# Kernel optimization log

Hardware: AMD Instinct MI355X
Metric: run time of the kernel (lower is better)

The kernel has to match this reference:

```python
import jax, jax.numpy as jnp
import numpy as np

N = 64
NUM_INPUTS = 6
NUM_OUTPUTS = 2
T_STEPS = 1024
BATCH = 1024
DT = 1.0
TAU = 10.0
ALPHA = DT / TAU
SIGMA_REC = 0.03
SIGMA_INP = 0.03
SLOPE = 1.0  # activation_slope for relu


def setup_inputs() -> dict:
    key = jax.random.key(0)
    k_u, k_rn, k_in, k_wi, k_wr, k_wo = jax.random.split(key, 6)
    u = jax.random.normal(k_u, (NUM_INPUTS, T_STEPS, BATCH), dtype=jnp.float32)
    rec_noise = jax.random.normal(k_rn, (N, T_STEPS, BATCH), dtype=jnp.float32)
    inp_noise = jax.random.normal(k_in, (NUM_INPUTS, T_STEPS, BATCH), dtype=jnp.float32)
    # learned params (masks are all-ones, already folded in)
    W_inp = jax.random.normal(k_wi, (N, NUM_INPUTS), dtype=jnp.float32) * 0.3
    W_rec = jax.random.normal(k_wr, (N, N), dtype=jnp.float32) * (0.9 / np.sqrt(N))
    W_out = jax.random.normal(k_wo, (NUM_OUTPUTS, N), dtype=jnp.float32) * 0.3
    return {"u": u, "rec_noise": rec_noise, "inp_noise": inp_noise,
            "W_inp": W_inp, "W_rec": W_rec, "W_out": W_out}


def _forward(u, rec_noise, inp_noise, W_inp, W_rec, W_out):
    # scale standard-normal noise exactly as torch: sqrt(2/alpha * sigma^2) * randn
    rn = jnp.sqrt(2.0 / ALPHA) * SIGMA_REC * rec_noise   # (N, T, B)
    inn = jnp.sqrt(2.0 / ALPHA) * SIGMA_INP * inp_noise  # (num_inputs, T, B)
    # move to (T, B, feat) for scan
    u_t = jnp.transpose(u, (1, 2, 0))     # (T, B, num_inputs)
    rn_t = jnp.transpose(rn, (1, 2, 0))   # (T, B, N)
    inn_t = jnp.transpose(inn, (1, 2, 0)) # (T, B, num_inputs)
    x0 = jnp.zeros((BATCH, N), dtype=u.dtype)  # self.x = zeros(N), broadcast over batch

    def step(x, inp):
        u_i, rn_i, in_i = inp
        pre = x @ W_rec.T + (u_i + in_i) @ W_inp.T
        act = jnp.maximum(0.0, SLOPE * pre)
        x_new = (1.0 - ALPHA) * x + ALPHA * (act + rn_i)
        return x_new, x_new

    # the torch loop runs T_steps-1 iterations using inputs at steps 0..T-2
    _, xs = jax.lax.scan(step, x0, (u_t[:-1], rn_t[:-1], inn_t[:-1]))
    states_tbn = jnp.concatenate([x0[None], xs], axis=0)  # (T, B, N)
    outputs_tbo = states_tbn @ W_out.T                    # (T, B, num_outputs)
    states = jnp.transpose(states_tbn, (2, 0, 1))   # (N, T, B)
    outputs = jnp.transpose(outputs_tbo, (2, 0, 1)) # (num_outputs, T, B)
    return states, outputs


def reference(u, rec_noise, inp_noise, W_inp, W_rec, W_out):
    return _forward(u, rec_noise, inp_noise, W_inp, W_rec, W_out)
```

## Files before the change

kernel.cpp:

```cpp
#include <hip/hip_runtime.h>

#define NN 64
#define NI 6
#define TT 1024
#define BB 1024
#define TB (TT * BB)
#define NSCALE 0.13416407864998738f
#define ARNSCALE 0.013416407864998739f
#define RREC 72
#define BSTRIDE (TT * RREC)

__device__ __forceinline__ float rdlane(float v, int l) {
    return __int_as_float(__builtin_amdgcn_readlane(__float_as_int(v), l));
}

__global__ __launch_bounds__(256) void build_rnu(
    const float* __restrict__ u,
    const float* __restrict__ rn,
    const float* __restrict__ inn,
    float* __restrict__ rnu)
{
    const int blk = blockIdx.x;
    const int t   = blk >> 4;
    const int b0  = (blk & 15) * 64;
    const int tid = threadIdx.x;

    __shared__ float lds[64][65];

    {
        const int c  = tid & 63;
        const int r0 = tid >> 6;
#pragma unroll
        for (int it = 0; it < 16; ++it) {
            const int n = 4 * it + r0;
            lds[c][n] = ARNSCALE * rn[n * TB + t * BB + b0 + c];
        }
    }
    __syncthreads();
    {
        const int cn = tid & 63;
        const int r0 = tid >> 6;
#pragma unroll
        for (int it = 0; it < 16; ++it) {
            const int r = 4 * it + r0;
            rnu[(b0 + r) * BSTRIDE + t * RREC + cn] = lds[r][cn];
        }
    }
    {
        const int i  = tid & 7;
        const int br = tid >> 3;
#pragma unroll
        for (int it = 0; it < 2; ++it) {
            const int b = br + 32 * it;
            float v = 0.0f;
            if (i < NI) {
                const int g = i * TB + t * BB + b0 + b;
                v = fmaf(NSCALE, inn[g], u[g]);
            }
            rnu[(b0 + b) * BSTRIDE + t * RREC + 64 + i] = v;
        }
    }
}

__global__ __launch_bounds__(64) void latent_rnn_lds(
    const float* __restrict__ rn_in,
    float* __restrict__ x_out,
    const float* __restrict__ Winp,
    const float* __restrict__ Wrec)
{
    const int hw = blockIdx.x;
    const int b  = (hw & 7) * 128 + (hw >> 3);
    const int n  = threadIdx.x;

    __shared__ __align__(16) float xs[2][80];

    float w[72];
#pragma unroll
    for (int k = 0; k < NN; k += 4) {
        const float4 w4 = *reinterpret_cast<const float4*>(Wrec + n * NN + k);
        w[k] = w4.x; w[k + 1] = w4.y; w[k + 2] = w4.z; w[k + 3] = w4.w;
    }
#pragma unroll
    for (int i = 0; i < NI; ++i) w[64 + i] = Winp[n * NI + i];
    w[70] = 0.0f; w[71] = 0.0f;

    const float* rptr = rn_in + b * BSTRIDE + n;
    const float* uptr = rn_in + b * BSTRIDE + 64 + (n & 7);
    float*       xdst = x_out + b * BSTRIDE + n;

    xs[0][n] = 0.0f;
    if (n < 8) xs[0][64 + n] = uptr[0];

    float rnb[4], utb[4];
#pragma unroll
    for (int d = 0; d < 4; ++d) {
        rnb[d] = rptr[d * RREC];
        utb[d] = uptr[(d + 1) * RREC];
    }

    float xreg = 0.0f;

#define STEP(tcur, slot, P)                                                   \
    do {                                                                      \
        const float rcur = rnb[slot];                                         \
        const float ucur = utb[slot];                         \
        { const int tp = ((tcur) + 4 < TT - 2) ? (tcur) + 4 : TT - 2;         \
          rnb[slot] = rptr[tp * RREC]; }                                      \
        { const int tq = ((tcur) + 5 < TT - 2) ? (tcur) + 5 : TT - 2;         \
          utb[slot] = uptr[tq * RREC]; }                                      \
        \
        const float4* row = reinterpret_cast<const float4*>(&xs[P][0]);       \
        float a0 = 0.f, a1 = 0.f, a2 = 0.f, a3 = 0.f;                         \
        _Pragma("unroll")                                                     \
        for (int q = 0; q < 18; ++q) {                                        \
            const float4 v = row[q];                                          \
            a0 = fmaf(v.x, w[4 * q + 0], a0);                                 \
            a1 = fmaf(v.y, w[4 * q + 1], a1);                                 \
            a2 = fmaf(v.z, w[4 * q + 2], a2);                                 \
            a3 = fmaf(v.w, w[4 * q + 3], a3);                                 \
        }                                                                     \
        const float pre = (a0 + a1) + (a2 + a3);                              \
        const float xn  = fmaf(0.9f, xreg,                                    \
                               fmaf(0.1f, fmaxf(pre, 0.f), rcur));            \
        xreg = xn;                                                            \
        xs[(P) ^ 1][n] = xn;                        \
        if (n < 8) xs[(P) ^ 1][64 + n] = ucur;                \
        xdst[(tcur) * RREC] = xn;                    \
    } while (0)

#pragma unroll 1
    for (int t = 0; t < 1020; t += 4) {
        STEP(t + 0, 0, 0);
        STEP(t + 1, 1, 1);
        STEP(t + 2, 2, 0);
        STEP(t + 3, 3, 1);
    }
    STEP(1020, 0, 0);
    STEP(1021, 1, 1);
    STEP(1022, 2, 0);
#undef STEP
}

__global__ __launch_bounds__(256) void trans_out(
    const float* __restrict__ rnu,
    const float* __restrict__ Wout,
    float* __restrict__ states,
    float* __restrict__ outputs)
{
    const int blk = blockIdx.x;
    const int t   = blk >> 4;
    const int b0  = (blk & 15) * 64;
    const int tid = threadIdx.x;

    __shared__ float xt[64][65];
    __shared__ float wo[2][64];

    if (tid < 128) wo[tid >> 6][tid & 63] = Wout[tid];

    const int col = tid & 63;
    const int r0  = tid >> 6;
    if (t == 0) {
#pragma unroll
        for (int it = 0; it < 16; ++it) xt[4 * it + r0][col] = 0.0f;
    } else {
#pragma unroll
        for (int it = 0; it < 16; ++it) {
            const int r = 4 * it + r0;
            xt[r][col] = rnu[(b0 + r) * BSTRIDE + (t - 1) * RREC + col];
        }
    }
    __syncthreads();

#pragma unroll
    for (int it = 0; it < 16; ++it) {
        const int n = 4 * it + r0;
        states[n * TB + t * BB + b0 + col] = xt[col][n];
    }

    if (tid < 128) {
        const int o  = tid >> 6;
        const int bb = tid & 63;
        float acc = 0.0f;
#pragma unroll
        for (int k = 0; k < NN; ++k) acc = fmaf(xt[bb][k], wo[o][k], acc);
        outputs[o * TB + t * BB + b0 + bb] = acc;
    }
}

#define BARRIER() do {                                                        \
    __builtin_amdgcn_sched_barrier(0);                                        \
    asm volatile("s_waitcnt lgkmcnt(0)\n\ts_barrier" ::: "memory");           \
    __builtin_amdgcn_sched_barrier(0);                                        \
} while (0)

__global__ __launch_bounds__(256, 1) void latent_rnn_fb(
    const float* __restrict__ u, const float* __restrict__ rn,
    const float* __restrict__ inn, const float* __restrict__ Winp,
    const float* __restrict__ Wrec, float* __restrict__ states)
{
    const int hw  = blockIdx.x;
    const int lb  = (hw & 7) * 32 + (hw >> 3);
    const int b0  = lb * 4;
    const int tid = threadIdx.x;
    const int l   = tid & 63;
    const int w   = tid >> 6;
    const int n   = tid >> 2;
    const int bs  = tid & 3;

    __shared__ float rnT[2][NN][5];
    __shared__ float xT[2][NN][5];
    __shared__ float iT[2][4][8];

    float wreg[NN];
#pragma unroll
    for (int k = 0; k < NN; k += 4) {
        const float4 w4 = *reinterpret_cast<const float4*>(Wrec + l * NN + k);
        wreg[k] = w4.x; wreg[k+1] = w4.y; wreg[k+2] = w4.z; wreg[k+3] = w4.w;
    }
    float wi[NI];
#pragma unroll
    for (int i = 0; i < NI; ++i) wi[i] = Winp[l * NI + i];

    const float* rsrc = rn + n * TB + b0 + bs;
    float*       sdst = states + n * TB + b0 + bs;
    const bool  ist  = (tid < NI * 4);
    const int   ii   = tid >> 2;
    const int   ib   = tid & 3;
    const float* usrc = u   + ii * TB + b0 + ib;
    const float* isrc = inn + ii * TB + b0 + ib;

    rnT[0][n][bs] = rsrc[0];
    if (ist) iT[0][ib][ii] = fmaf(NSCALE, isrc[0], usrc[0]);
    xT[0][l][w] = 0.0f;

    float rnPF[4], uPF[4], iPF[4];
#pragma unroll
    for (int d = 0; d < 4; ++d) {
        rnPF[d] = rsrc[(d + 1) * BB];
        if (ist) { uPF[d] = usrc[(d + 1) * BB]; iPF[d] = isrc[(d + 1) * BB]; }
    }
    __syncthreads();

    float xreg = 0.0f;

#define FSTEP(tcur, slot, CC)                                                 \
  {                                                                           \
    sdst[(tcur) * BB] = xT[CC][n][bs];                                        \
    const float rcur = rnT[CC][l][w];                                         \
    const float4 iv0 = *reinterpret_cast<const float4*>(&iT[CC][w][0]);       \
    const float2 iv1 = *reinterpret_cast<const float2*>(&iT[CC][w][4]);       \
    float a0 = 0.f, a1 = 0.f, a2 = 0.f, a3 = 0.f;                             \
    _Pragma("unroll")                                                         \
    for (int k = 0; k < NN; k += 4) {                                         \
        a0 = fmaf(rdlane(xreg, k + 0), wreg[k + 0], a0);                      \
        a1 = fmaf(rdlane(xreg, k + 1), wreg[k + 1], a1);                      \
        a2 = fmaf(rdlane(xreg, k + 2), wreg[k + 2], a2);                      \
        a3 = fmaf(rdlane(xreg, k + 3), wreg[k + 3], a3);                      \
    }                                                                         \
    a0 = fmaf(iv0.x, wi[0], a0); a1 = fmaf(iv0.y, wi[1], a1);                 \
    a2 = fmaf(iv0.z, wi[2], a2); a3 = fmaf(iv0.w, wi[3], a3);                 \
    a0 = fmaf(iv1.x, wi[4], a0); a1 = fmaf(iv1.y, wi[5], a1);                 \
    const float pre = (a0 + a1) + (a2 + a3);                                  \
    const float xn  = fmaf(0.9f, xreg,                                        \
                           fmaf(0.1f, fmaxf(pre, 0.f), ARNSCALE * rcur));     \
    xreg = xn;                                                                \
    xT[(CC) ^ 1][l][w] = xn;                                                  \
    rnT[(CC) ^ 1][n][bs] = rnPF[slot];                                        \
    if (ist) iT[(CC) ^ 1][ib][ii] = fmaf(NSCALE, iPF[slot], uPF[slot]);       \
    { int tp = (tcur) + 5; if (tp > TT - 2) tp = TT - 2;                      \
      rnPF[slot] = rsrc[tp * BB];                                             \
      if (ist) { uPF[slot] = usrc[tp * BB]; iPF[slot] = isrc[tp * BB]; } }    \
    BARRIER();                                                                \
  }

#pragma unroll 1
    for (int t = 0; t < 1020; t += 4) {
        FSTEP(t + 0, 0, 0);
        FSTEP(t + 1, 1, 1);
        FSTEP(t + 2, 2, 0);
        FSTEP(t + 3, 3, 1);
    }
    FSTEP(1020, 0, 0);
    FSTEP(1021, 1, 1);
    FSTEP(1022, 2, 0);
#undef FSTEP

    sdst[(TT - 1) * BB] = xT[1][n][bs];
}

__global__ __launch_bounds__(256) void out_proj(
    const float* __restrict__ states,
    const float* __restrict__ Wout,
    float* __restrict__ outputs)
{
    const int g4 = (blockIdx.x * 256 + threadIdx.x) * 4;
    float4 a0 = {0.f, 0.f, 0.f, 0.f};
    float4 a1 = {0.f, 0.f, 0.f, 0.f};
#pragma unroll
    for (int k = 0; k < NN; ++k) {
        const float4 s = *reinterpret_cast<const float4*>(states + k * TB + g4);
        const float w0 = Wout[k];
        const float w1 = Wout[NN + k];
        a0.x = fmaf(s.x, w0, a0.x); a0.y = fmaf(s.y, w0, a0.y);
        a0.z = fmaf(s.z, w0, a0.z); a0.w = fmaf(s.w, w0, a0.w);
        a1.x = fmaf(s.x, w1, a1.x); a1.y = fmaf(s.y, w1, a1.y);
        a1.z = fmaf(s.z, w1, a1.z); a1.w = fmaf(s.w, w1, a1.w);
    }
    *reinterpret_cast<float4*>(outputs + g4)      = a0;
    *reinterpret_cast<float4*>(outputs + TB + g4) = a1;
}

extern "C" void kernel_launch(void* const* d_in, const int* in_sizes, int n_in,
                              void* d_out, int out_size, void* d_ws, size_t ws_size,
                              hipStream_t stream) {
    const float* u    = (const float*)d_in[0];
    const float* rn   = (const float*)d_in[1];
    const float* inn  = (const float*)d_in[2];
    const float* Winp = (const float*)d_in[3];
    const float* Wrec = (const float*)d_in[4];
    const float* Wout = (const float*)d_in[5];

    float* states  = (float*)d_out;
    float* outputs = (float*)d_out + (size_t)NN * TT * BB;

    const size_t need = (size_t)BB * TT * RREC * sizeof(float);
    if (ws_size >= need) {
        float* rnu = (float*)d_ws;
        build_rnu<<<TT * 16, 256, 0, stream>>>(u, rn, inn, rnu);
        latent_rnn_lds<<<1024, 64, 0, stream>>>(rnu, rnu, Winp, Wrec);
        trans_out<<<TT * 16, 256, 0, stream>>>(rnu, Wout, states, outputs);
    } else {
        latent_rnn_fb<<<256, 256, 0, stream>>>(u, rn, inn, Winp, Wrec, states);
        out_proj<<<1024, 256, 0, stream>>>(states, Wout, outputs);
    }
}
```

Measured before the change: 694.4 us.

## Process two batch rows per wavefront with two neurons per lane in RNN scan

```diff
diff --git a/kernel.cpp b/kernel.cpp
--- a/kernel.cpp
+++ b/kernel.cpp
@@ -62,70 +62,86 @@
     }
 }
 
-__global__ __launch_bounds__(64) void latent_rnn_lds(
+__global__ __launch_bounds__(64, 1) void latent_rnn_2b(
     const float* __restrict__ rn_in,
     float* __restrict__ x_out,
     const float* __restrict__ Winp,
     const float* __restrict__ Wrec)
 {
     const int hw = blockIdx.x;
-    const int b  = (hw & 7) * 128 + (hw >> 3);
-    const int n  = threadIdx.x;
-
-    __shared__ __align__(16) float xs[2][80];
-
-    float w[72];
+    const int g  = (hw & 7) * 64 + (hw >> 3);
+    const int b0 = g * 2;
+    const int l  = threadIdx.x;
+    const int h  = l >> 5;
+    const int p  = l & 31;
+    const int n0 = 2 * p;
+    const int bb = b0 + h;
+
+    __shared__ __align__(16) float xs[2][2][88];
+
+    float w0[72], w1[72];
 #pragma unroll
     for (int k = 0; k < NN; k += 4) {
-        const float4 w4 = *reinterpret_cast<const float4*>(Wrec + n * NN + k);
-        w[k] = w4.x; w[k + 1] = w4.y; w[k + 2] = w4.z; w[k + 3] = w4.w;
-    }
-#pragma unroll
-    for (int i = 0; i < NI; ++i) w[64 + i] = Winp[n * NI + i];
-    w[70] = 0.0f; w[71] = 0.0f;
-
-    const float* rptr = rn_in + b * BSTRIDE + n;
-    const float* uptr = rn_in + b * BSTRIDE + 64 + (n & 7);
-    float*       xdst = x_out + b * BSTRIDE + n;
-
-    xs[0][n] = 0.0f;
-    if (n < 8) xs[0][64 + n] = uptr[0];
-
-    float rnb[4], utb[4];
+        const float4 a = *reinterpret_cast<const float4*>(Wrec + n0 * NN + k);
+        const float4 b = *reinterpret_cast<const float4*>(Wrec + (n0 + 1) * NN + k);
+        w0[k] = a.x; w0[k+1] = a.y; w0[k+2] = a.z; w0[k+3] = a.w;
+        w1[k] = b.x; w1[k+1] = b.y; w1[k+2] = b.z; w1[k+3] = b.w;
+    }
+#pragma unroll
+    for (int i = 0; i < NI; ++i) {
+        w0[64 + i] = Winp[n0 * NI + i];
+        w1[64 + i] = Winp[(n0 + 1) * NI + i];
+    }
+    w0[70] = 0.f; w0[71] = 0.f; w1[70] = 0.f; w1[71] = 0.f;
+#pragma unroll
+    for (int k = 0; k < 72; ++k) asm volatile("" : "+v"(w0[k]));
+#pragma unroll
+    for (int k = 0; k < 72; ++k) asm volatile("" : "+v"(w1[k]));
+
+    const float* rptr = rn_in + bb * BSTRIDE + n0;
+    const float* uptr = rn_in + bb * BSTRIDE + 64 + (p & 7);
+    float*       xdst = x_out + bb * BSTRIDE + n0;
+
+    *reinterpret_cast<float2*>(&xs[h][0][n0]) = make_float2(0.f, 0.f);
+    if (p < 8) xs[h][0][64 + p] = uptr[0];
+
+    float2 rnb[4];
+    float  utb[4];
 #pragma unroll
     for (int d = 0; d < 4; ++d) {
-        rnb[d] = rptr[d * RREC];
+        rnb[d] = *reinterpret_cast<const float2*>(rptr + d * RREC);
         utb[d] = uptr[(d + 1) * RREC];
     }
 
-    float xreg = 0.0f;
+    float x0 = 0.0f, x1 = 0.0f;
 
 #define STEP(tcur, slot, P)                                                   \
     do {                                                                      \
-        const float rcur = rnb[slot];                                         \
-        const float ucur = utb[slot];                         \
+        const float2 rcur = rnb[slot];                                        \
+        const float  ucur = utb[slot];                                        \
         { const int tp = ((tcur) + 4 < TT - 2) ? (tcur) + 4 : TT - 2;         \
-          rnb[slot] = rptr[tp * RREC]; }                                      \
+          rnb[slot] = *reinterpret_cast<const float2*>(rptr + tp * RREC); }   \
         { const int tq = ((tcur) + 5 < TT - 2) ? (tcur) + 5 : TT - 2;         \
           utb[slot] = uptr[tq * RREC]; }                                      \
-        \
-        const float4* row = reinterpret_cast<const float4*>(&xs[P][0]);       \
+        const float4* row = reinterpret_cast<const float4*>(&xs[h][P][0]);    \
         float a0 = 0.f, a1 = 0.f, a2 = 0.f, a3 = 0.f;                         \
+        float c0 = 0.f, c1 = 0.f, c2 = 0.f, c3 = 0.f;                         \
         _Pragma("unroll")                                                     \
         for (int q = 0; q < 18; ++q) {                                        \
             const float4 v = row[q];                                          \
-            a0 = fmaf(v.x, w[4 * q + 0], a0);                                 \
-            a1 = fmaf(v.y, w[4 * q + 1], a1);                                 \
-            a2 = fmaf(v.z, w[4 * q + 2], a2);                                 \
-            a3 = fmaf(v.w, w[4 * q + 3], a3);                                 \
+            a0 = fmaf(v.x, w0[4*q+0], a0); c0 = fmaf(v.x, w1[4*q+0], c0);     \
+            a1 = fmaf(v.y, w0[4*q+1], a1); c1 = fmaf(v.y, w1[4*q+1], c1);     \
+            a2 = fmaf(v.z, w0[4*q+2], a2); c2 = fmaf(v.z, w1[4*q+2], c2);     \
+            a3 = fmaf(v.w, w0[4*q+3], a3); c3 = fmaf(v.w, w1[4*q+3], c3);     \
         }                                                                     \
-        const float pre = (a0 + a1) + (a2 + a3);                              \
-        const float xn  = fmaf(0.9f, xreg,                                    \
-                               fmaf(0.1f, fmaxf(pre, 0.f), rcur));            \
-        xreg = xn;                                                            \
-        xs[(P) ^ 1][n] = xn;                        \
-        if (n < 8) xs[(P) ^ 1][64 + n] = ucur;                \
-        xdst[(tcur) * RREC] = xn;                    \
+        const float pre0 = (a0 + a1) + (a2 + a3);                             \
+        const float pre1 = (c0 + c1) + (c2 + c3);                             \
+        const float xn0 = fmaf(0.9f, x0, fmaf(0.1f, fmaxf(pre0, 0.f), rcur.x)); \
+        const float xn1 = fmaf(0.9f, x1, fmaf(0.1f, fmaxf(pre1, 0.f), rcur.y)); \
+        x0 = xn0; x1 = xn1;                                                   \
+        *reinterpret_cast<float2*>(&xs[h][(P) ^ 1][n0]) = make_float2(xn0, xn1); \
+        if (p < 8) xs[h][(P) ^ 1][64 + p] = ucur;                             \
+        *reinterpret_cast<float2*>(xdst + (tcur) * RREC) = make_float2(xn0, xn1); \
     } while (0)
 
 #pragma unroll 1
@@ -327,7 +343,7 @@
     if (ws_size >= need) {
         float* rnu = (float*)d_ws;
         build_rnu<<<TT * 16, 256, 0, stream>>>(u, rn, inn, rnu);
-        latent_rnn_lds<<<1024, 64, 0, stream>>>(rnu, rnu, Winp, Wrec);
+        latent_rnn_2b<<<512, 64, 0, stream>>>(rnu, rnu, Winp, Wrec);
         trans_out<<<TT * 16, 256, 0, stream>>>(rnu, Wout, states, outputs);
     } else {
         latent_rnn_fb<<<256, 256, 0, stream>>>(u, rn, inn, Winp, Wrec, states);
```

After: 775.0 us. 11.6% more time.

## Split recurrent dot product across wave halves with cross-lane shuffle

Applied to the files above, without the earlier changes.

```diff
diff --git a/kernel.cpp b/kernel.cpp
--- a/kernel.cpp
+++ b/kernel.cpp
@@ -62,7 +62,7 @@
     }
 }
 
-__global__ __launch_bounds__(64) void latent_rnn_lds(
+__global__ __launch_bounds__(64, 1) void latent_rnn_split(
     const float* __restrict__ rn_in,
     float* __restrict__ x_out,
     const float* __restrict__ Winp,
@@ -71,18 +71,24 @@
     const int hw = blockIdx.x;
     const int b  = (hw & 7) * 128 + (hw >> 3);
     const int n  = threadIdx.x;
+    const int h  = n >> 5;
+    const int hb = 32 * h;
+    const int np = n ^ 32;
 
     __shared__ __align__(16) float xs[2][80];
 
-    float w[72];
-#pragma unroll
-    for (int k = 0; k < NN; k += 4) {
-        const float4 w4 = *reinterpret_cast<const float4*>(Wrec + n * NN + k);
-        w[k] = w4.x; w[k + 1] = w4.y; w[k + 2] = w4.z; w[k + 3] = w4.w;
-    }
-#pragma unroll
-    for (int i = 0; i < NI; ++i) w[64 + i] = Winp[n * NI + i];
-    w[70] = 0.0f; w[71] = 0.0f;
+    float ws[32], wp[32];
+#pragma unroll
+    for (int j = 0; j < 32; j += 4) {
+        const float4 a = *reinterpret_cast<const float4*>(Wrec + n  * NN + hb + j);
+        const float4 c = *reinterpret_cast<const float4*>(Wrec + np * NN + hb + j);
+        ws[j] = a.x; ws[j+1] = a.y; ws[j+2] = a.z; ws[j+3] = a.w;
+        wp[j] = c.x; wp[j+1] = c.y; wp[j+2] = c.z; wp[j+3] = c.w;
+    }
+    float wu[8];
+#pragma unroll
+    for (int i = 0; i < NI; ++i) wu[i] = Winp[n * NI + i];
+    wu[6] = 0.0f; wu[7] = 0.0f;
 
     const float* rptr = rn_in + b * BSTRIDE + n;
     const float* uptr = rn_in + b * BSTRIDE + 64 + (n & 7);
@@ -108,18 +114,28 @@
           rnb[slot] = rptr[tp * RREC]; }                                      \
         { const int tq = ((tcur) + 5 < TT - 2) ? (tcur) + 5 : TT - 2;         \
           utb[slot] = uptr[tq * RREC]; }                                      \
-        \
-        const float4* row = reinterpret_cast<const float4*>(&xs[P][0]);       \
-        float a0 = 0.f, a1 = 0.f, a2 = 0.f, a3 = 0.f;                         \
+                                             \
+        const float4* xrow = reinterpret_cast<const float4*>(&xs[P][hb]);     \
+        float a0 = 0.f, a1 = 0.f;                 \
+        float c0 = 0.f, c1 = 0.f;              \
         _Pragma("unroll")                                                     \
-        for (int q = 0; q < 18; ++q) {                                        \
-            const float4 v = row[q];                                          \
-            a0 = fmaf(v.x, w[4 * q + 0], a0);                                 \
-            a1 = fmaf(v.y, w[4 * q + 1], a1);                                 \
-            a2 = fmaf(v.z, w[4 * q + 2], a2);                                 \
-            a3 = fmaf(v.w, w[4 * q + 3], a3);                                 \
+        for (int q = 0; q < 8; ++q) {                                         \
+            const float4 v = xrow[q];                                         \
+            a0 = fmaf(v.x, ws[4*q+0], a0); c0 = fmaf(v.x, wp[4*q+0], c0);     \
+            a1 = fmaf(v.y, ws[4*q+1], a1); c1 = fmaf(v.y, wp[4*q+1], c1);     \
+            a0 = fmaf(v.z, ws[4*q+2], a0); c0 = fmaf(v.z, wp[4*q+2], c0);     \
+            a1 = fmaf(v.w, ws[4*q+3], a1); c1 = fmaf(v.w, wp[4*q+3], c1);     \
         }                                                                     \
-        const float pre = (a0 + a1) + (a2 + a3);                              \
+                                 \
+        const float4 iv0 = *reinterpret_cast<const float4*>(&xs[P][64]);      \
+        const float4 iv1 = *reinterpret_cast<const float4*>(&xs[P][68]);      \
+        a0 = fmaf(iv0.x, wu[0], a0); a1 = fmaf(iv0.y, wu[1], a1);             \
+        a0 = fmaf(iv0.z, wu[2], a0); a1 = fmaf(iv0.w, wu[3], a1);             \
+        a0 = fmaf(iv1.x, wu[4], a0); a1 = fmaf(iv1.y, wu[5], a1);             \
+                   \
+        const float p2 = c0 + c1;                                             \
+        const float pr = __shfl_xor(p2, 32);                                  \
+        const float pre = (a0 + a1) + pr;                                     \
         const float xn  = fmaf(0.9f, xreg,                                    \
                                fmaf(0.1f, fmaxf(pre, 0.f), rcur));            \
         xreg = xn;                                                            \
@@ -327,7 +343,7 @@
     if (ws_size >= need) {
         float* rnu = (float*)d_ws;
         build_rnu<<<TT * 16, 256, 0, stream>>>(u, rn, inn, rnu);
-        latent_rnn_lds<<<1024, 64, 0, stream>>>(rnu, rnu, Winp, Wrec);
+        latent_rnn_split<<<1024, 64, 0, stream>>>(rnu, rnu, Winp, Wrec);
         trans_out<<<TT * 16, 256, 0, stream>>>(rnu, Wout, states, outputs);
     } else {
         latent_rnn_fb<<<256, 256, 0, stream>>>(u, rn, inn, Winp, Wrec, states);
```

Measured after the change: 625.8 us. 1.11x faster.

## Split recurrent dot product into quarter partials combined with cross-lane shuffles

Applied to the files above, without the earlier changes.

```diff
diff --git a/kernel.cpp b/kernel.cpp
--- a/kernel.cpp
+++ b/kernel.cpp
@@ -62,7 +62,7 @@
     }
 }
 
-__global__ __launch_bounds__(64) void latent_rnn_lds(
+__global__ __launch_bounds__(64, 1) void latent_rnn_quart(
     const float* __restrict__ rn_in,
     float* __restrict__ x_out,
     const float* __restrict__ Winp,
@@ -71,18 +71,33 @@
     const int hw = blockIdx.x;
     const int b  = (hw & 7) * 128 + (hw >> 3);
     const int n  = threadIdx.x;
+    const int q  = (n >> 4) & 3;
+    const int qb = 16 * q;
 
     __shared__ __align__(16) float xs[2][80];
 
-    float w[72];
-#pragma unroll
-    for (int k = 0; k < NN; k += 4) {
-        const float4 w4 = *reinterpret_cast<const float4*>(Wrec + n * NN + k);
-        w[k] = w4.x; w[k + 1] = w4.y; w[k + 2] = w4.z; w[k + 3] = w4.w;
-    }
-#pragma unroll
-    for (int i = 0; i < NI; ++i) w[64 + i] = Winp[n * NI + i];
-    w[70] = 0.0f; w[71] = 0.0f;
+    const int r0 = n, r1 = n ^ 16, r2 = n ^ 32, r3 = n ^ 48;
+    float w0[16], w1[16], w2[16], w3[16];
+#pragma unroll
+    for (int j = 0; j < 16; j += 4) {
+        const float4 a = *reinterpret_cast<const float4*>(Wrec + r0 * NN + qb + j);
+        const float4 c = *reinterpret_cast<const float4*>(Wrec + r1 * NN + qb + j);
+        const float4 d = *reinterpret_cast<const float4*>(Wrec + r2 * NN + qb + j);
+        const float4 e = *reinterpret_cast<const float4*>(Wrec + r3 * NN + qb + j);
+        w0[j] = a.x; w0[j+1] = a.y; w0[j+2] = a.z; w0[j+3] = a.w;
+        w1[j] = c.x; w1[j+1] = c.y; w1[j+2] = c.z; w1[j+3] = c.w;
+        w2[j] = d.x; w2[j+1] = d.y; w2[j+2] = d.z; w2[j+3] = d.w;
+        w3[j] = e.x; w3[j+1] = e.y; w3[j+2] = e.z; w3[j+3] = e.w;
+    }
+    float u0[2], u1[2], u2[2], u3[2];
+#pragma unroll
+    for (int j = 0; j < 2; ++j) {
+        const int i = 2 * q + j;
+        u0[j] = (i < NI) ? Winp[r0 * NI + i] : 0.0f;
+        u1[j] = (i < NI) ? Winp[r1 * NI + i] : 0.0f;
+        u2[j] = (i < NI) ? Winp[r2 * NI + i] : 0.0f;
+        u3[j] = (i < NI) ? Winp[r3 * NI + i] : 0.0f;
+    }
 
     const float* rptr = rn_in + b * BSTRIDE + n;
     const float* uptr = rn_in + b * BSTRIDE + 64 + (n & 7);
@@ -99,6 +114,21 @@
     }
 
     float xreg = 0.0f;
+
+#define DOT4(P, W, UW)                                                        \
+    do {                                                                      \
+        float pa = 0.f, pb = 0.f;                                             \
+        pa = fmaf(v0.x, W[0],  pa); pb = fmaf(v0.y, W[1],  pb);               \
+        pa = fmaf(v0.z, W[2],  pa); pb = fmaf(v0.w, W[3],  pb);               \
+        pa = fmaf(v1.x, W[4],  pa); pb = fmaf(v1.y, W[5],  pb);               \
+        pa = fmaf(v1.z, W[6],  pa); pb = fmaf(v1.w, W[7],  pb);               \
+        pa = fmaf(v2.x, W[8],  pa); pb = fmaf(v2.y, W[9],  pb);               \
+        pa = fmaf(v2.z, W[10], pa); pb = fmaf(v2.w, W[11], pb);               \
+        pa = fmaf(v3.x, W[12], pa); pb = fmaf(v3.y, W[13], pb);               \
+        pa = fmaf(v3.z, W[14], pa); pb = fmaf(v3.w, W[15], pb);               \
+        pa = fmaf(uv.x, UW[0], pa); pb = fmaf(uv.y, UW[1], pb);               \
+        P = pa + pb;                                                          \
+    } while (0)
 
 #define STEP(tcur, slot, P)                                                   \
     do {                                                                      \
@@ -106,20 +136,24 @@
         const float ucur = utb[slot];                         \
         { const int tp = ((tcur) + 4 < TT - 2) ? (tcur) + 4 : TT - 2;         \
           rnb[slot] = rptr[tp * RREC]; }                                      \
-        { const int tq = ((tcur) + 5 < TT - 2) ? (tcur) + 5 : TT - 2;         \
-          utb[slot] = uptr[tq * RREC]; }                                      \
+        { const int tq2 = ((tcur) + 5 < TT - 2) ? (tcur) + 5 : TT - 2;        \
+          utb[slot] = uptr[tq2 * RREC]; }                                     \
         \
-        const float4* row = reinterpret_cast<const float4*>(&xs[P][0]);       \
-        float a0 = 0.f, a1 = 0.f, a2 = 0.f, a3 = 0.f;                         \
-        _Pragma("unroll")                                                     \
-        for (int q = 0; q < 18; ++q) {                                        \
-            const float4 v = row[q];                                          \
-            a0 = fmaf(v.x, w[4 * q + 0], a0);                                 \
-            a1 = fmaf(v.y, w[4 * q + 1], a1);                                 \
-            a2 = fmaf(v.z, w[4 * q + 2], a2);                                 \
-            a3 = fmaf(v.w, w[4 * q + 3], a3);                                 \
-        }                                                                     \
-        const float pre = (a0 + a1) + (a2 + a3);                              \
+        const float4* xrow = reinterpret_cast<const float4*>(&xs[P][qb]);     \
+        const float4 v0 = xrow[0];                                            \
+        const float4 v1 = xrow[1];                                            \
+        const float4 v2 = xrow[2];                                            \
+        const float4 v3 = xrow[3];                                            \
+        const float2 uv = *reinterpret_cast<const float2*>(&xs[P][64 + 2*q]); \
+        float P0, P1, P2, P3;                                                 \
+        DOT4(P0, w0, u0);                                                     \
+        DOT4(P1, w1, u1);                                                     \
+        DOT4(P2, w2, u2);                                                     \
+        DOT4(P3, w3, u3);                                                     \
+                                         \
+        const float A = P0 + __shfl_xor(P1, 16);                              \
+        const float Bp = P2 + __shfl_xor(P3, 16);                             \
+        const float pre = A + __shfl_xor(Bp, 32);                             \
         const float xn  = fmaf(0.9f, xreg,                                    \
                                fmaf(0.1f, fmaxf(pre, 0.f), rcur));            \
         xreg = xn;                                                            \
@@ -139,6 +173,7 @@
     STEP(1021, 1, 1);
     STEP(1022, 2, 0);
 #undef STEP
+#undef DOT4
 }
 
 __global__ __launch_bounds__(256) void trans_out(
@@ -327,7 +362,7 @@
     if (ws_size >= need) {
         float* rnu = (float*)d_ws;
         build_rnu<<<TT * 16, 256, 0, stream>>>(u, rn, inn, rnu);
-        latent_rnn_lds<<<1024, 64, 0, stream>>>(rnu, rnu, Winp, Wrec);
+        latent_rnn_quart<<<1024, 64, 0, stream>>>(rnu, rnu, Winp, Wrec);
         trans_out<<<TT * 16, 256, 0, stream>>>(rnu, Wout, states, outputs);
     } else {
         latent_rnn_fb<<<256, 256, 0, stream>>>(u, rn, inn, Winp, Wrec, states);
```

Measured after the change: 636.0 us. -8.4%, faster.
